# Optimization experiments

Hardware: AMD Instinct MI355X
Metric: run time of the kernel (lower is better)

## Reference

```python
import jax, jax.numpy as jnp
import numpy as np

TOKENS, IN_F, OUT_F, R = 16384, 4096, 4096, 16
ALPHA = 32.0
SCALING = ALPHA / R  # 2.0
BITS = 8
QMAX = 2 ** (BITS - 1) - 1   # 127
QMIN = -2 ** (BITS - 1)      # -128


def setup_inputs() -> dict:
    key = jax.random.key(0)
    k1, k2, k3, k4 = jax.random.split(key, 4)
    x = jax.random.normal(k1, (TOKENS, IN_F), dtype=jnp.float32)
    weight = jax.random.normal(k2, (OUT_F, IN_F), dtype=jnp.float32) * 0.02
    lora_a = jax.random.normal(k3, (IN_F, R), dtype=jnp.float32) * 0.02
    lora_b = jax.random.normal(k4, (R, OUT_F), dtype=jnp.float32) * 0.02
    return {"x": x, "weight": weight, "lora_a": lora_a, "lora_b": lora_b}


def _quant_dequant(w):
    # Symmetric per-output-row (last-axis) absmax int8 quantize then dequantize.
    abs_max = jnp.max(jnp.abs(w), axis=-1, keepdims=True)      # [out, 1]
    scale = abs_max / QMAX
    w_q = jnp.clip(jnp.round(w / (scale + 1e-8)), QMIN, QMAX)
    return w_q * scale


def reference(x, weight, lora_a, lora_b):
    w = _quant_dequant(weight)                                  # [out, in]
    out = jnp.dot(x, w.T)                                       # [T, out]
    lora = jnp.dot(jnp.dot(x, lora_a), lora_b)                  # [T, r] -> [T, out]
    return out + SCALING * lora
```

## Files before the change

### kernel.cpp

```cpp
#include <hip/hip_runtime.h>
#include <stdint.h>

typedef __attribute__((ext_vector_type(4))) float f32x4;
typedef __attribute__((ext_vector_type(8))) short s16x8;
typedef __attribute__((ext_vector_type(4))) int i32x4;

#define TOKENS 16384
#define IN_F 4096
#define OUT_F 4096
#define RNK 16
#define BM 256
#define BN 256
#define BKB 128
#define NTILE (IN_F / BKB)

static __device__ __forceinline__ unsigned short f32_to_bf16(float f) {
    uint32_t u = __builtin_bit_cast(uint32_t, f);
    uint32_t r = (u + 0x7FFFu + ((u >> 16) & 1u)) >> 16;
    return (unsigned short)r;
}

static __device__ __forceinline__ void direct_load16(const void* g, void* l) {
    __builtin_amdgcn_global_load_lds(
        (const __attribute__((address_space(1))) void*)(uintptr_t)g,
        (__attribute__((address_space(3))) void*)(uintptr_t)l,
        16, 0, 0);
}

static __device__ __forceinline__ i32x4 mfma_i8(i32x4 a, i32x4 b, i32x4 c) {
    return __builtin_amdgcn_mfma_i32_16x16x64_i8(a, b, c, 0, 0, 0);
}
static __device__ __forceinline__ f32x4 mfma16(s16x8 a, s16x8 b, f32x4 c) {
    return __builtin_amdgcn_mfma_f32_16x16x32_bf16(a, b, c, 0, 0, 0);
}

#define BAR() asm volatile("s_barrier" ::: "memory")
#define VM(n) asm volatile("s_waitcnt vmcnt(" #n ")" ::: "memory")
#define SB0() __builtin_amdgcn_sched_barrier(0)

__global__ __launch_bounds__(256) void qd_weight_kernel(const float* __restrict__ w,
                                                        const float* __restrict__ lb,
                                                        uint32_t* __restrict__ wq,
                                                        float* __restrict__ wscale,
                                                        unsigned short* __restrict__ lbt) {
    const int row = blockIdx.x;
    const int tid = threadIdx.x;
    const float* wr = w + (size_t)row * IN_F;
    f32x4 v[4];
#pragma unroll
    for (int p = 0; p < 4; ++p)
        v[p] = *(const f32x4*)(wr + (size_t)(tid + p * 256) * 4);
    float m = 0.f;
#pragma unroll
    for (int p = 0; p < 4; ++p)
#pragma unroll
        for (int e = 0; e < 4; ++e)
            m = fmaxf(m, fabsf(v[p][e]));
#pragma unroll
    for (int off = 1; off < 64; off <<= 1)
        m = fmaxf(m, __shfl_xor(m, off, 64));
    __shared__ float red[4];
    if ((tid & 63) == 0) red[tid >> 6] = m;
    __syncthreads();
    m = fmaxf(fmaxf(red[0], red[1]), fmaxf(red[2], red[3]));
    const float scale = m * (1.0f / 127.0f);
    const float denom = scale + 1e-8f;
#pragma unroll
    for (int p = 0; p < 4; ++p) {
        uint32_t pack = 0;
#pragma unroll
        for (int e = 0; e < 4; ++e) {
            float q = rintf(v[p][e] / denom);
            q = fminf(fmaxf(q, -128.f), 127.f);
            pack |= ((uint32_t)(uint8_t)(int)q) << (8 * e);
        }
        wq[(size_t)row * (IN_F / 4) + tid + p * 256] = pack;
    }
    if (tid == 0) wscale[row] = scale;
    if (tid < RNK)
        lbt[(size_t)row * RNK + tid] = f32_to_bf16(lb[(size_t)tid * OUT_F + row]);
}

__global__ __launch_bounds__(256) void laq_kernel(const float* __restrict__ la,
                                                  char* __restrict__ laqT,
                                                  float* __restrict__ lascale) {
    const int r = blockIdx.x;
    const int tid = threadIdx.x;
    float v[16];
#pragma unroll
    for (int j = 0; j < 16; ++j)
        v[j] = la[(size_t)(tid + j * 256) * RNK + r];
    float m = 0.f;
#pragma unroll
    for (int j = 0; j < 16; ++j) m = fmaxf(m, fabsf(v[j]));
#pragma unroll
    for (int off = 1; off < 64; off <<= 1)
        m = fmaxf(m, __shfl_xor(m, off, 64));
    __shared__ float red[4];
    if ((tid & 63) == 0) red[tid >> 6] = m;
    __syncthreads();
    m = fmaxf(fmaxf(red[0], red[1]), fmaxf(red[2], red[3]));
    m = fmaxf(m, 1e-12f);
    const float inv = 127.0f / m;
    if (tid == 0) lascale[r] = m * (1.0f / 127.0f);
#pragma unroll
    for (int j = 0; j < 16; ++j) {
        float q = fminf(fmaxf(rintf(v[j] * inv), -128.f), 127.f);
        laqT[(size_t)r * IN_F + tid + j * 256] = (char)(int)q;
    }
}

__global__ __launch_bounds__(256) void xquant_kernel(const float* __restrict__ x,
                                                     uint32_t* __restrict__ xqw,
                                                     float* __restrict__ xscale) {
    const int lane = threadIdx.x & 63;
    const int t = blockIdx.x * 4 + (threadIdx.x >> 6);
    const float* xr = x + (size_t)t * IN_F;

    f32x4 xv[16];
#pragma unroll
    for (int j = 0; j < 16; ++j)
        xv[j] = *(const f32x4*)(xr + j * 256 + lane * 4);

    float m = 0.f;
#pragma unroll
    for (int j = 0; j < 16; ++j)
#pragma unroll
        for (int e = 0; e < 4; ++e) m = fmaxf(m, fabsf(xv[j][e]));
#pragma unroll
    for (int off = 1; off < 64; off <<= 1)
        m = fmaxf(m, __shfl_xor(m, off, 64));
    m = fmaxf(m, 1e-6f);
    const float inv = 127.0f / m;
    if (lane == 0) xscale[t] = m * (1.0f / 127.0f);

#pragma unroll
    for (int j = 0; j < 16; ++j) {
        uint32_t pack = 0;
#pragma unroll
        for (int e = 0; e < 4; ++e) {
            float q = fminf(fmaxf(rintf(xv[j][e] * inv), -128.f), 127.f);
            pack |= ((uint32_t)(uint8_t)(int)q) << (8 * e);
        }
        xqw[(size_t)t * (IN_F / 4) + j * 64 + lane] = pack;
    }
}

__global__ __launch_bounds__(256) void lora_t_kernel(const char* __restrict__ xq,
                                                     const char* __restrict__ laqT,
                                                     const float* __restrict__ xscale,
                                                     const float* __restrict__ lascale,
                                                     unsigned short* __restrict__ tbf) {
    const int tid = threadIdx.x;
    const int lane = tid & 63;
    const int wid = tid >> 6;
    const int t0 = blockIdx.x * 64 + wid * 16;
    const int lrow = lane & 15;
    const int lko = lane >> 4;

    const char* pA = xq + (size_t)(t0 + lrow) * IN_F + lko * 16;
    const char* pB = laqT + (size_t)lrow * IN_F + lko * 16;

    i32x4 acc = {0, 0, 0, 0};
#pragma unroll 8
    for (int it = 0; it < IN_F / 64; ++it) {
        i32x4 a = *(const i32x4*)(pA + it * 64);
        i32x4 b = *(const i32x4*)(pB + it * 64);
        acc = mfma_i8(a, b, acc);
    }

    const float ls = lascale[lrow];
    const f32x4 xs = *(const f32x4*)(xscale + t0 + lko * 4);
#pragma unroll
    for (int q = 0; q < 4; ++q)
        tbf[(size_t)(t0 + lko * 4 + q) * RNK + lrow] =
            f32_to_bf16(2.0f * xs[q] * ls * (float)acc[q]);
}

__global__ __launch_bounds__(512, 2) void gemm8p_i8_kernel(const char* __restrict__ xq,
                                                           const char* __restrict__ wq,
                                                           const float* __restrict__ xscale,
                                                           const float* __restrict__ wscale,
                                                           const unsigned short* __restrict__ tbf,
                                                           const unsigned short* __restrict__ lbt,
                                                           float* __restrict__ out) {
    __shared__ char lds[131072];

    const int bid = blockIdx.x;
    const int swz = (bid & 7) * 128 + (bid >> 3);
    const int tm = swz & 63, tn = swz >> 6;
    const int brow = tm * BM, bcol = tn * BN;

    const int tid = threadIdx.x;
    const int lane = tid & 63;
    const int wid = tid >> 6;
    const int wm = wid >> 2, wn = wid & 3;
    const int lrow = lane & 15;
    const int lko = lane >> 4;

    const int s_r = tid >> 3;
    const int scb = ((tid & 7) * 16) ^ (((tid >> 3) & 7) << 4);
    const char* gA = xq + (size_t)(brow + s_r) * IN_F + scb;
    const char* gB = wq + (size_t)(bcol + s_r) * IN_F + scb;

    char* const sA0 = (char*)lds;
    char* const sA1 = (char*)lds + 32768;
    char* const sB0 = (char*)lds + 65536;
    char* const sB1 = (char*)lds + 98304;

    const int aBase = (wm * 128 + lrow) * 128;
    const int bBase = (wn * 64 + lrow) * 128;
    const int koff[2] = {(lko * 16) ^ ((lrow & 7) << 4),
                         ((lko * 16) | 64) ^ ((lrow & 7) << 4)};

    i32x4 acc[8][4];
#pragma unroll
    for (int mf = 0; mf < 8; ++mf)
#pragma unroll
        for (int nf = 0; nf < 4; ++nf)
#pragma unroll
            for (int q = 0; q < 4; ++q) acc[mf][nf][q] = 0;

#define STAGE_A(kk, base, half)                                                                       \
    do {                                                                                              \
        direct_load16(gA + (size_t)((half) * 128) * IN_F + (kk), (base) + (half) * 16384 + tid * 16); \
        direct_load16(gA + (size_t)((half) * 128 + 64) * IN_F + (kk),                                 \
                      (base) + (half) * 16384 + 8192 + tid * 16);                                     \
    } while (0)
#define STAGE_B(kk, base, half)                                                                       \
    do {                                                                                              \
        direct_load16(gB + (size_t)((half) * 128) * IN_F + (kk), (base) + (half) * 16384 + tid * 16); \
        direct_load16(gB + (size_t)((half) * 128 + 64) * IN_F + (kk),                                 \
                      (base) + (half) * 16384 + 8192 + tid * 16);                                     \
    } while (0)

#define READ_AL(Ab)                                                          \
    _Pragma("unroll") for (int mf = 0; mf < 4; ++mf) {                       \
        aL[mf][0] = *(const i32x4*)((Ab) + aBase + mf * 2048 + koff[0]);     \
        aL[mf][1] = *(const i32x4*)((Ab) + aBase + mf * 2048 + koff[1]);     \
    }
#define READ_AH(Ab)                                                               \
    _Pragma("unroll") for (int mf = 0; mf < 4; ++mf) {                            \
        aH[mf][0] = *(const i32x4*)((Ab) + aBase + (4 + mf) * 2048 + koff[0]);    \
        aH[mf][1] = *(const i32x4*)((Ab) + aBase + (4 + mf) * 2048 + koff[1]);    \
    }
#define READ_BL(Bb)                                                          \
    _Pragma("unroll") for (int nf = 0; nf < 2; ++nf) {                       \
        bL[nf][0] = *(const i32x4*)((Bb) + bBase + nf * 2048 + koff[0]);     \
        bL[nf][1] = *(const i32x4*)((Bb) + bBase + nf * 2048 + koff[1]);     \
    }
#define READ_BH(Bb)                                                               \
    _Pragma("unroll") for (int nf = 0; nf < 2; ++nf) {                            \
        bH[nf][0] = *(const i32x4*)((Bb) + bBase + (2 + nf) * 2048 + koff[0]);    \
        bH[nf][1] = *(const i32x4*)((Bb) + bBase + (2 + nf) * 2048 + koff[1]);    \
    }
#define QUAD(MB, NB, AF, BF)                                                  \
    do {                                                                      \
        _Pragma("unroll") for (int mf = 0; mf < 4; ++mf)                      \
            _Pragma("unroll") for (int nf = 0; nf < 2; ++nf) {                \
            acc[(MB) + mf][(NB) + nf] =                                       \
                mfma_i8(AF[mf][0], BF[nf][0], acc[(MB) + mf][(NB) + nf]);     \
            acc[(MB) + mf][(NB) + nf] =                                       \
                mfma_i8(AF[mf][1], BF[nf][1], acc[(MB) + mf][(NB) + nf]);     \
        }                                                                     \
    } while (0)

    STAGE_A(0, sA0, 0);
    STAGE_A(0, sA0, 1);
    STAGE_B(0, sB0, 0);
    STAGE_B(0, sB0, 1);
    STAGE_B(BKB, sB1, 0);
    STAGE_B(BKB, sB1, 1);
    VM(4);
    BAR();

    i32x4 aL[4][2], aH[4][2], bL[2][2], bH[2][2];

    for (int i = 0; i < NTILE / 2; ++i) {
        const int t = 2 * i;
        const int kk1 = (t + 1) * BKB, kk2 = (t + 2) * BKB, kk3 = (t + 3) * BKB;
        const bool pf = (t + 2 < NTILE);

        READ_AL(sA0);
        READ_BL(sB0);
        STAGE_A(kk1, sA1, 0);
        QUAD(0, 0, aL, bL);
        READ_BH(sB0);
        STAGE_A(kk1, sA1, 1);
        QUAD(0, 2, aL, bH);
        SB0();
        BAR();

        READ_AH(sA0);
        if (pf) STAGE_B(kk2, sB0, 0);
        QUAD(4, 2, aH, bH);
        if (pf) {
            STAGE_B(kk2, sB0, 1);
            VM(4);
        } else {
            VM(0);
        }
        SB0();
        BAR();
        QUAD(4, 0, aH, bL);

        READ_AL(sA1);
        READ_BL(sB1);
        if (pf) STAGE_A(kk2, sA0, 0);
        QUAD(0, 0, aL, bL);
        READ_BH(sB1);
        if (pf) STAGE_A(kk2, sA0, 1);
        QUAD(0, 2, aL, bH);
        SB0();
        BAR();

        READ_AH(sA1);
        if (pf) STAGE_B(kk3, sB1, 0);
        QUAD(4, 2, aH, bH);
        if (pf) STAGE_B(kk3, sB1, 1);
        VM(4);
        SB0();
        BAR();
        QUAD(4, 0, aH, bL);
    }
#undef STAGE_A
#undef STAGE_B
#undef READ_AL
#undef READ_AH
#undef READ_BL
#undef READ_BH
#undef QUAD

    __syncthreads();
    unsigned short* tls = (unsigned short*)lds;
    unsigned short* lls = (unsigned short*)(lds + 8192);
    {
        const int row = tid >> 1, h = tid & 1;
        *(s16x8*)(tls + row * 16 + h * 8) = *(const s16x8*)(tbf + (size_t)(brow + row) * RNK + h * 8);
        *(s16x8*)(lls + row * 16 + h * 8) = *(const s16x8*)(lbt + (size_t)(bcol + row) * RNK + h * 8);
    }
    __syncthreads();

    const int c0 = bcol + wn * 64 + lrow;
    const int r0base = brow + wm * 128 + lko * 4;

    s16x8 z;
#pragma unroll
    for (int e = 0; e < 8; ++e) z[e] = 0;
    s16x8 at8[8], bl8[4];
#pragma unroll
    for (int mf = 0; mf < 8; ++mf) {
        const int row = wm * 128 + mf * 16 + lrow;
        at8[mf] = (lko < 2) ? *(const s16x8*)(tls + row * 16 + lko * 8) : z;
    }
#pragma unroll
    for (int nf = 0; nf < 4; ++nf) {
        const int row = wn * 64 + nf * 16 + lrow;
        bl8[nf] = (lko < 2) ? *(const s16x8*)(lls + row * 16 + lko * 8) : z;
    }
    float ws4[4];
#pragma unroll
    for (int nf = 0; nf < 4; ++nf) ws4[nf] = wscale[c0 + nf * 16];

    const f32x4 zf = {0.f, 0.f, 0.f, 0.f};
#pragma unroll
    for (int mf = 0; mf < 8; ++mf) {
        f32x4 lor[4];
#pragma unroll
        for (int nf = 0; nf < 4; ++nf) lor[nf] = mfma16(at8[mf], bl8[nf], zf);
        const f32x4 xs4 = *(const f32x4*)(xscale + r0base + mf * 16);
#pragma unroll
        for (int q = 0; q < 4; ++q) {
            float* orow = out + (size_t)(r0base + mf * 16 + q) * OUT_F;
#pragma unroll
            for (int nf = 0; nf < 4; ++nf)
                orow[c0 + nf * 16] =
                    xs4[q] * ws4[nf] * (float)acc[mf][nf][q] + lor[nf][q];
        }
    }
}

extern "C" void kernel_launch(void* const* d_in, const int* in_sizes, int n_in,
                              void* d_out, int out_size, void* d_ws, size_t ws_size,
                              hipStream_t stream) {
    const float* x  = (const float*)d_in[0];
    const float* w  = (const float*)d_in[1];
    const float* la = (const float*)d_in[2];
    const float* lb = (const float*)d_in[3];
    float* out = (float*)d_out;

    char* ws = (char*)d_ws;
    size_t off = 0;
    char* xq = ws + off;                 off += (size_t)TOKENS * IN_F;
    char* wqb = ws + off;                off += (size_t)OUT_F * IN_F;
    unsigned short* tbf = (unsigned short*)(ws + off); off += (size_t)TOKENS * RNK * 2;
    unsigned short* lbt = (unsigned short*)(ws + off); off += (size_t)OUT_F * RNK * 2;
    float* xscale = (float*)(ws + off);  off += (size_t)TOKENS * 4;
    float* wscale = (float*)(ws + off);  off += (size_t)OUT_F * 4;
    char* laqT = ws + off;               off += (size_t)RNK * IN_F;
    float* lascale = (float*)(ws + off); off += RNK * 4;

    qd_weight_kernel<<<OUT_F, 256, 0, stream>>>(w, lb, (uint32_t*)wqb, wscale, lbt);
    laq_kernel<<<RNK, 256, 0, stream>>>(la, laqT, lascale);
    xquant_kernel<<<TOKENS / 4, 256, 0, stream>>>(x, (uint32_t*)xq, xscale);
    lora_t_kernel<<<TOKENS / 64, 256, 0, stream>>>(xq, laqT, xscale, lascale, tbf);
    gemm8p_i8_kernel<<<(TOKENS / BM) * (OUT_F / BN), 512, 0, stream>>>(
        xq, wqb, xscale, wscale, tbf, lbt, out);
}
```

Measured before the change: 381.4 us.

## Load weight B fragments directly from global into registers, skipping LDS staging

Weight tiles were staged through LDS with double buffering. Now each wave loads its B fragments straight from global memory into registers, and only A goes through LDS, which halves LDS use to 64KB. The main loop becomes a simpler single-tile body. The cost is that B is no longer shared through LDS: the four waves sharing a column read it redundantly from global/L2, the global load latency is exposed per tile, and the B loads now happen in the same step as the barrier.

```diff
diff --git a/kernel.cpp b/kernel.cpp
--- a/kernel.cpp
+++ b/kernel.cpp
@@ -177,14 +177,14 @@
             f32_to_bf16(2.0f * xs[q] * ls * (float)acc[q]);
 }
 
-__global__ __launch_bounds__(512, 2) void gemm8p_i8_kernel(const char* __restrict__ xq,
-                                                           const char* __restrict__ wq,
-                                                           const float* __restrict__ xscale,
-                                                           const float* __restrict__ wscale,
-                                                           const unsigned short* __restrict__ tbf,
-                                                           const unsigned short* __restrict__ lbt,
-                                                           float* __restrict__ out) {
-    __shared__ char lds[131072];
+__global__ __launch_bounds__(512, 2) void gemm_i8_bdirect_kernel(const char* __restrict__ xq,
+                                                                 const char* __restrict__ wq,
+                                                                 const float* __restrict__ xscale,
+                                                                 const float* __restrict__ wscale,
+                                                                 const unsigned short* __restrict__ tbf,
+                                                                 const unsigned short* __restrict__ lbt,
+                                                                 float* __restrict__ out) {
+    __shared__ char lds[65536];
 
     const int bid = blockIdx.x;
     const int swz = (bid & 7) * 128 + (bid >> 3);
@@ -201,17 +201,15 @@
     const int s_r = tid >> 3;
     const int scb = ((tid & 7) * 16) ^ (((tid >> 3) & 7) << 4);
     const char* gA = xq + (size_t)(brow + s_r) * IN_F + scb;
-    const char* gB = wq + (size_t)(bcol + s_r) * IN_F + scb;
 
     char* const sA0 = (char*)lds;
     char* const sA1 = (char*)lds + 32768;
-    char* const sB0 = (char*)lds + 65536;
-    char* const sB1 = (char*)lds + 98304;
 
     const int aBase = (wm * 128 + lrow) * 128;
-    const int bBase = (wn * 64 + lrow) * 128;
     const int koff[2] = {(lko * 16) ^ ((lrow & 7) << 4),
                          ((lko * 16) | 64) ^ ((lrow & 7) << 4)};
+
+    const char* gBf = wq + (size_t)(bcol + wn * 64 + lrow) * IN_F + lko * 16;
 
     i32x4 acc[8][4];
 #pragma unroll
@@ -227,12 +225,6 @@
         direct_load16(gA + (size_t)((half) * 128 + 64) * IN_F + (kk),                                 \
                       (base) + (half) * 16384 + 8192 + tid * 16);                                     \
     } while (0)
-#define STAGE_B(kk, base, half)                                                                       \
-    do {                                                                                              \
-        direct_load16(gB + (size_t)((half) * 128) * IN_F + (kk), (base) + (half) * 16384 + tid * 16); \
-        direct_load16(gB + (size_t)((half) * 128 + 64) * IN_F + (kk),                                 \
-                      (base) + (half) * 16384 + 8192 + tid * 16);                                     \
-    } while (0)
 
 #define READ_AL(Ab)                                                          \
     _Pragma("unroll") for (int mf = 0; mf < 4; ++mf) {                       \
@@ -244,16 +236,17 @@
         aH[mf][0] = *(const i32x4*)((Ab) + aBase + (4 + mf) * 2048 + koff[0]);    \
         aH[mf][1] = *(const i32x4*)((Ab) + aBase + (4 + mf) * 2048 + koff[1]);    \
     }
-#define READ_BL(Bb)                                                          \
-    _Pragma("unroll") for (int nf = 0; nf < 2; ++nf) {                       \
-        bL[nf][0] = *(const i32x4*)((Bb) + bBase + nf * 2048 + koff[0]);     \
-        bL[nf][1] = *(const i32x4*)((Bb) + bBase + nf * 2048 + koff[1]);     \
-    }
-#define READ_BH(Bb)                                                               \
-    _Pragma("unroll") for (int nf = 0; nf < 2; ++nf) {                            \
-        bH[nf][0] = *(const i32x4*)((Bb) + bBase + (2 + nf) * 2048 + koff[0]);    \
-        bH[nf][1] = *(const i32x4*)((Bb) + bBase + (2 + nf) * 2048 + koff[1]);    \
-    }
+#define LOAD_B(kk)                                                                         \
+    do {                                                                                   \
+        _Pragma("unroll") for (int nf = 0; nf < 2; ++nf) {                                 \
+            bL[nf][0] = *(const i32x4*)(gBf + (size_t)(nf * 16) * IN_F + (kk));            \
+            bL[nf][1] = *(const i32x4*)(gBf + (size_t)(nf * 16) * IN_F + (kk) + 64);       \
+        }                                                                                  \
+        _Pragma("unroll") for (int nf = 0; nf < 2; ++nf) {                                 \
+            bH[nf][0] = *(const i32x4*)(gBf + (size_t)((2 + nf) * 16) * IN_F + (kk));      \
+            bH[nf][1] = *(const i32x4*)(gBf + (size_t)((2 + nf) * 16) * IN_F + (kk) + 64); \
+        }                                                                                  \
+    } while (0)
 #define QUAD(MB, NB, AF, BF)                                                  \
     do {                                                                      \
         _Pragma("unroll") for (int mf = 0; mf < 4; ++mf)                      \
@@ -265,70 +258,47 @@
         }                                                                     \
     } while (0)
 
+    i32x4 aL[4][2], aH[4][2], bL[2][2], bH[2][2];
+
     STAGE_A(0, sA0, 0);
     STAGE_A(0, sA0, 1);
-    STAGE_B(0, sB0, 0);
-    STAGE_B(0, sB0, 1);
-    STAGE_B(BKB, sB1, 0);
-    STAGE_B(BKB, sB1, 1);
+    LOAD_B(0);
+    STAGE_A(BKB, sA1, 0);
+    STAGE_A(BKB, sA1, 1);
     VM(4);
     BAR();
 
-    i32x4 aL[4][2], aH[4][2], bL[2][2], bH[2][2];
+#define TILE_BODY(t, Acur)                                                    \
+    do {                                                                      \
+        const int kk1 = ((t) + 1) * BKB, kk2 = ((t) + 2) * BKB;               \
+        READ_AL(Acur);                                                        \
+        QUAD(0, 0, aL, bL);                                                   \
+        QUAD(0, 2, aL, bH);                                                   \
+        READ_AH(Acur);                                                        \
+        QUAD(4, 2, aH, bH);                                                   \
+        QUAD(4, 0, aH, bL);                                                   \
+        if ((t) + 1 < NTILE) LOAD_B(kk1);                                     \
+        SB0();                                                                \
+        BAR();                               \
+        if ((t) + 2 < NTILE) {                                                \
+            STAGE_A(kk2, Acur, 0);                                            \
+            STAGE_A(kk2, Acur, 1);                                            \
+            VM(4);              \
+        } else {                                                              \
+            VM(0);                             \
+        }                                                                     \
+        BAR();                                                \
+    } while (0)
 
     for (int i = 0; i < NTILE / 2; ++i) {
-        const int t = 2 * i;
-        const int kk1 = (t + 1) * BKB, kk2 = (t + 2) * BKB, kk3 = (t + 3) * BKB;
-        const bool pf = (t + 2 < NTILE);
-
-        READ_AL(sA0);
-        READ_BL(sB0);
-        STAGE_A(kk1, sA1, 0);
-        QUAD(0, 0, aL, bL);
-        READ_BH(sB0);
-        STAGE_A(kk1, sA1, 1);
-        QUAD(0, 2, aL, bH);
-        SB0();
-        BAR();
-
-        READ_AH(sA0);
-        if (pf) STAGE_B(kk2, sB0, 0);
-        QUAD(4, 2, aH, bH);
-        if (pf) {
-            STAGE_B(kk2, sB0, 1);
-            VM(4);
-        } else {
-            VM(0);
-        }
-        SB0();
-        BAR();
-        QUAD(4, 0, aH, bL);
-
-        READ_AL(sA1);
-        READ_BL(sB1);
-        if (pf) STAGE_A(kk2, sA0, 0);
-        QUAD(0, 0, aL, bL);
-        READ_BH(sB1);
-        if (pf) STAGE_A(kk2, sA0, 1);
-        QUAD(0, 2, aL, bH);
-        SB0();
-        BAR();
-
-        READ_AH(sA1);
-        if (pf) STAGE_B(kk3, sB1, 0);
-        QUAD(4, 2, aH, bH);
-        if (pf) STAGE_B(kk3, sB1, 1);
-        VM(4);
-        SB0();
-        BAR();
-        QUAD(4, 0, aH, bL);
-    }
+        TILE_BODY(2 * i, sA0);
+        TILE_BODY(2 * i + 1, sA1);
+    }
+#undef TILE_BODY
 #undef STAGE_A
-#undef STAGE_B
 #undef READ_AL
 #undef READ_AH
-#undef READ_BL
-#undef READ_BH
+#undef LOAD_B
 #undef QUAD
 
     __syncthreads();
@@ -404,6 +374,6 @@
     laq_kernel<<<RNK, 256, 0, stream>>>(la, laqT, lascale);
     xquant_kernel<<<TOKENS / 4, 256, 0, stream>>>(x, (uint32_t*)xq, xscale);
     lora_t_kernel<<<TOKENS / 64, 256, 0, stream>>>(xq, laqT, xscale, lascale, tbf);
-    gemm8p_i8_kernel<<<(TOKENS / BM) * (OUT_F / BN), 512, 0, stream>>>(
+    gemm_i8_bdirect_kernel<<<(TOKENS / BM) * (OUT_F / BN), 512, 0, stream>>>(
         xq, wqb, xscale, wscale, tbf, lbt, out);
 }
```

Result: slower. 522.3 us (+37.0%).
